# Kernel optimization log

Measured on AMD Instinct MI355X. Metric: run time of the kernel, lower is better.

## Reference

```python
import jax, jax.numpy as jnp
import numpy as np

H = 8          # n_heads
C_FACTOR = 3   # autocorrelation factor c
KS = 25        # series-decomp moving-average kernel


def series_decomp(x, ks=KS):
    # AvgPool1d(kernel=ks, stride=1, pad=ks//2), count_include_pad=True (torch default)
    p = ks // 2
    xp = jnp.pad(x, ((0, 0), (p, p), (0, 0)))            # [B, L+2p, D]
    cs = jnp.pad(jnp.cumsum(xp, axis=1), ((0, 0), (1, 0), (0, 0)))
    trend = (cs[:, ks:, :] - cs[:, :-ks, :]) / ks         # [B, L, D]
    return x - trend, trend


def auto_correlation(x, Wq, bq, Wk, bk, Wv, bv):
    B, L, D = x.shape
    d = D // H

    def proj(W, b):  # [B,L,D] -> [B,H,L,d]
        return (x @ W + b).reshape(B, L, H, d).transpose(0, 2, 1, 3)

    Q, K, V = proj(Wq, bq), proj(Wk, bk), proj(Wv, bv)
    Qf = jnp.fft.rfft(Q, axis=2)
    Kf = jnp.fft.rfft(K, axis=2)
    Corr = jnp.fft.irfft(Qf * jnp.conj(Kf), n=L, axis=2)  # [B,H,L,d]

    k = int(C_FACTOR * np.log(L))                         # topk = int(c*log(L))
    C2 = Corr.transpose(0, 1, 3, 2)                       # [B,H,d,L] - topk along lag axis per channel
    W_topk, I_topk = jax.lax.top_k(C2, k)                 # [B,H,d,k]
    W_topk = jax.nn.softmax(W_topk, axis=-1)

    # saturating shift: pos = min(delay + t, L-1)  (faithful to clamp(max=L-1))
    t = jnp.arange(L)
    pos = jnp.minimum(I_topk[..., None] + t[None, None, None, None, :], L - 1)  # [B,H,d,k,L]
    Vt = V.transpose(0, 1, 3, 2)                          # [B,H,d,L]
    gathered = jnp.take_along_axis(Vt[:, :, :, None, :], pos, axis=4)           # [B,H,d,k,L]
    R = jnp.einsum('bhdk,bhdkl->bhdl', W_topk, gathered)  # weighted aggregate over lags
    return R.transpose(0, 3, 1, 2).reshape(B, L, D)       # [B,L,D]


def setup_inputs() -> dict:
    key = jax.random.key(0)
    ks = jax.random.split(key, 11)
    B, L, D = 8, 1024, 512
    s = 0.02
    return {
        'x':  jax.random.normal(ks[0], (B, L, D), jnp.float32),
        'Wq': jax.random.normal(ks[1], (D, D), jnp.float32) * s,
        'bq': jnp.zeros((D,), jnp.float32),
        'Wk': jax.random.normal(ks[2], (D, D), jnp.float32) * s,
        'bk': jnp.zeros((D,), jnp.float32),
        'Wv': jax.random.normal(ks[3], (D, D), jnp.float32) * s,
        'bv': jnp.zeros((D,), jnp.float32),
        'W1': jax.random.normal(ks[4], (D, D), jnp.float32) * s,
        'b1': jnp.zeros((D,), jnp.float32),
        'W2': jax.random.normal(ks[5], (D, D), jnp.float32) * s,
        'b2': jnp.zeros((D,), jnp.float32),
    }


def reference(x, Wq, bq, Wk, bk, Wv, bv, W1, b1, W2, b2):
    attn = auto_correlation(x, Wq, bq, Wk, bk, Wv, bv)
    x_s, _ = series_decomp(attn + x)
    y = jax.nn.relu(x_s @ W1 + b1) @ W2 + b2              # FFN (dropout is identity in eval)
    x_s, _ = series_decomp(y + x_s)
    return x_s
```

## Files before the change

### kernel.cpp

```cpp
#include <hip/hip_runtime.h>
#include <math.h>

#define LL 1024
#define DD 512
#define NB 8
#define KTOP 20
#define SZ (8 * 512 * 1024)

typedef __attribute__((ext_vector_type(8))) short bf16x8;
typedef __attribute__((ext_vector_type(4))) float f32x4;
typedef __attribute__((ext_vector_type(4))) int i32x4;

__device__ __forceinline__ unsigned short f2bf(float f) {
  union { float f; unsigned u; } v; v.f = f;
  unsigned r = v.u + 0x7FFFu + ((v.u >> 16) & 1u);
  return (unsigned short)(r >> 16);
}
__device__ __forceinline__ float bf2f(unsigned short u) {
  union { unsigned u; float f; } v; v.u = ((unsigned)u) << 16;
  return v.f;
}

__device__ __forceinline__ void gload16(const void* g, void* l) {
  __builtin_amdgcn_global_load_lds(
      (const __attribute__((address_space(1))) unsigned int*)g,
      (__attribute__((address_space(3))) unsigned int*)l, 16, 0, 0);
}

__global__ __launch_bounds__(256) void k_prep(const float* __restrict__ x,
                                              unsigned short* __restrict__ xbT,
                                              unsigned short* __restrict__ xb,
                                              const float* __restrict__ Wq,
                                              const float* __restrict__ Wk,
                                              const float* __restrict__ Wv,
                                              const float* __restrict__ W1,
                                              const float* __restrict__ W2,
                                              const float* __restrict__ bq,
                                              const float* __restrict__ bk,
                                              const float* __restrict__ bv,
                                              unsigned short* __restrict__ WqkvT,
                                              unsigned short* __restrict__ W1T,
                                              unsigned short* __restrict__ W2T,
                                              float* __restrict__ bqkv) {
  __shared__ float T[64][65];
  int bid = blockIdx.x;
  int tid = threadIdx.x;
  int lane = tid & 63, r4 = tid >> 6;
  if (bid < 1024) {
    int b = bid >> 7, c0 = ((bid >> 4) & 7) * 64, t0 = (bid & 15) * 64;
#pragma unroll
    for (int it = 0; it < 16; ++it) {
      int tl = it * 4 + r4;
      T[lane][tl] = x[((size_t)b * LL + t0 + tl) * DD + c0 + lane];
    }
    __syncthreads();
#pragma unroll
    for (int it = 0; it < 16; ++it) {
      int cl = it * 4 + r4;
      xbT[((size_t)b * DD + c0 + cl) * LL + t0 + lane] = f2bf(T[cl][lane]);
    }
    int tl2 = tid >> 2, cq = (tid & 3) * 16;
    unsigned short* dxb = xb + ((size_t)b * LL + t0 + tl2) * DD + c0 + cq;
#pragma unroll
    for (int j = 0; j < 16; j += 4) {
      ushort4 u;
      u.x = f2bf(T[cq + j][tl2]);
      u.y = f2bf(T[cq + j + 1][tl2]);
      u.z = f2bf(T[cq + j + 2][tl2]);
      u.w = f2bf(T[cq + j + 3][tl2]);
      *(ushort4*)&dxb[j] = u;
    }
  } else {
    int pid = bid - 1024;
    int z = pid >> 6, n0 = ((pid >> 3) & 7) * 64, k0 = (pid & 7) * 64;
    const float* W = (z == 0) ? Wq : (z == 1) ? Wk : (z == 2) ? Wv : (z == 3) ? W1 : W2;
    unsigned short* dst = (z == 0) ? WqkvT
                        : (z == 1) ? (WqkvT + 512 * 512)
                        : (z == 2) ? (WqkvT + 1024 * 512)
                        : (z == 3) ? W1T : W2T;
#pragma unroll
    for (int it = 0; it < 16; ++it) {
      int kl = it * 4 + r4;
      T[lane][kl] = W[(size_t)(k0 + kl) * DD + n0 + lane];
    }
    __syncthreads();
    int n = tid >> 2, kq = (tid & 3) * 16;
    unsigned short* d = dst + (size_t)(n0 + n) * DD + k0 + kq;
#pragma unroll
    for (int j = 0; j < 16; j += 4) {
      ushort4 u;
      u.x = f2bf(T[n][kq + j]);
      u.y = f2bf(T[n][kq + j + 1]);
      u.z = f2bf(T[n][kq + j + 2]);
      u.w = f2bf(T[n][kq + j + 3]);
      *(ushort4*)&d[j] = u;
    }
    if (z == 4 && n0 == 0 && k0 == 0) {
      for (int i = tid; i < 1536; i += 256) {
        const float* s = (i < 512) ? bq : (i < 1024) ? bk : bv;
        bqkv[i] = s[i & 511];
      }
    }
  }
}

template <int MODE>
__global__ __launch_bounds__(256) void k_mfma(const unsigned short* __restrict__ Aptr,
                                              const unsigned short* __restrict__ Bt,
                                              const float* __restrict__ bias,
                                              const unsigned short* __restrict__ resbT,
                                              unsigned short* __restrict__ outU,
                                              float* __restrict__ outF, int gx) {
  __shared__ char smem[34816];
  unsigned short* As = (unsigned short*)smem;
  unsigned short* Bs = (unsigned short*)(smem + 16384);
  float* Cs = (float*)smem;

  int tid = threadIdx.x;
  int lane = tid & 63, wid = tid >> 6;
  int wr = wid & 1, wc = wid >> 1;

  int nwg = gridDim.x;
  int wg = blockIdx.x;
  int swz = (wg & 7) * (nwg >> 3) + (wg >> 3);
  int bix = swz % gx, biy = swz / gx;
  int n0 = bix * 128, m0 = biy * 128;
  int b = m0 >> 10, t0 = m0 & (LL - 1);

  f32x4 acc[4][4];
#pragma unroll
  for (int i = 0; i < 4; ++i)
#pragma unroll
    for (int j = 0; j < 4; ++j) acc[i][j] = (f32x4){0.f, 0.f, 0.f, 0.f};

  int srow = tid >> 3, sq = tid & 7;

  for (int k0 = 0; k0 < 512; k0 += 64) {
#pragma unroll
    for (int p = 0; p < 4; ++p) {
      int r = srow + p * 32;
      int dq = sq ^ (r & 7);
      gload16(Aptr + (size_t)(m0 + r) * 512 + k0 + dq * 8, &As[r * 64 + sq * 8]);
      gload16(Bt + (size_t)(n0 + r) * 512 + k0 + dq * 8, &Bs[r * 64 + sq * 8]);
    }
    __syncthreads();
#pragma unroll
    for (int ks = 0; ks < 2; ++ks) {
      bf16x8 af[4], bf[4];
      int fr = lane & 15, kq = lane >> 4;
#pragma unroll
      for (int mi = 0; mi < 4; ++mi) {
        int r = wr * 64 + mi * 16 + fr;
        af[mi] = *(bf16x8*)&As[r * 64 + ((ks * 4 + kq) ^ (r & 7)) * 8];
      }
#pragma unroll
      for (int ni = 0; ni < 4; ++ni) {
        int r = wc * 64 + ni * 16 + fr;
        bf[ni] = *(bf16x8*)&Bs[r * 64 + ((ks * 4 + kq) ^ (r & 7)) * 8];
      }
#pragma unroll
      for (int mi = 0; mi < 4; ++mi)
#pragma unroll
        for (int ni = 0; ni < 4; ++ni)
          acc[mi][ni] = __builtin_amdgcn_mfma_f32_16x16x32_bf16(af[mi], bf[ni], acc[mi][ni], 0, 0, 0);
    }
    __syncthreads();
  }

  if (MODE == 0 || MODE == 2) {
    const int LDc = 132;
    for (int p = 0; p < 2; ++p) {
      __syncthreads();
      if (MODE == 2) {
        int n = tid >> 2, mq = tid & 3;
        const unsigned short* rrow =
            resbT + ((size_t)(b * 512) + n0 + p * 64 + n) * LL + t0;
#pragma unroll
        for (int i = 0; i < 8; ++i) {
          int m = mq * 4 + i * 16;
          ushort4 u = *(const ushort4*)&rrow[m];
          float4 v;
          v.x = bf2f(u.x); v.y = bf2f(u.y); v.z = bf2f(u.z); v.w = bf2f(u.w);
          *(float4*)&Cs[n * LDc + m] = v;
        }
        __syncthreads();
      }
      if (wc == p) {
#pragma unroll
        for (int mi = 0; mi < 4; ++mi)
#pragma unroll
          for (int ni = 0; ni < 4; ++ni) {
            int nl = ni * 16 + (lane & 15);
            int ml = wr * 64 + mi * 16 + (lane >> 4) * 4;
            if (MODE == 2) {
              f32x4 cur = *(f32x4*)&Cs[nl * LDc + ml];
              cur += acc[mi][ni];
              *(f32x4*)&Cs[nl * LDc + ml] = cur;
            } else {
              *(f32x4*)&Cs[nl * LDc + ml] = acc[mi][ni];
            }
          }
      }
      __syncthreads();
      {
        int n = tid >> 2, mq = tid & 3;
        int ng = n0 + p * 64 + n;
        float bv = bias[ng];
        if (MODE == 0) {
          int sel = ng >> 9;
          unsigned short* drow =
              outU + ((size_t)sel * NB * 512 + b * 512 + (ng & 511)) * LL + t0;
#pragma unroll
          for (int i = 0; i < 8; ++i) {
            int m = mq * 4 + i * 16;
            float4 v = *(float4*)&Cs[n * LDc + m];
            ushort4 u;
            u.x = f2bf(v.x + bv); u.y = f2bf(v.y + bv);
            u.z = f2bf(v.z + bv); u.w = f2bf(v.w + bv);
            *(ushort4*)&drow[m] = u;
          }
        } else {
          float* drow = outF + ((size_t)b * 512 + ng) * LL + t0;
#pragma unroll
          for (int i = 0; i < 8; ++i) {
            int m = mq * 4 + i * 16;
            float4 v = *(float4*)&Cs[n * LDc + m];
            v.x += bv; v.y += bv; v.z += bv; v.w += bv;
            *(float4*)&drow[m] = v;
          }
        }
      }
    }
  } else {
    const int LDh = 68;
    for (int p = 0; p < 2; ++p) {
      __syncthreads();
      if (wc == p) {
#pragma unroll
        for (int mi = 0; mi < 4; ++mi)
#pragma unroll
          for (int ni = 0; ni < 4; ++ni) {
            int nl = ni * 16 + (lane & 15);
            int ml = wr * 64 + mi * 16 + (lane >> 4) * 4;
#pragma unroll
            for (int r = 0; r < 4; ++r) Cs[(ml + r) * LDh + nl] = acc[mi][ni][r];
          }
      }
      __syncthreads();
      {
        int m = tid >> 1, nh = tid & 1;
        unsigned short* drow =
            outU + (size_t)(m0 + m) * 512 + n0 + p * 64 + nh * 32;
#pragma unroll
        for (int c = 0; c < 8; ++c) {
          float4 v = *(float4*)&Cs[m * LDh + nh * 32 + c * 4];
          float4 bb = *(const float4*)&bias[n0 + p * 64 + nh * 32 + c * 4];
          v.x = fmaxf(v.x + bb.x, 0.f);
          v.y = fmaxf(v.y + bb.y, 0.f);
          v.z = fmaxf(v.z + bb.z, 0.f);
          v.w = fmaxf(v.w + bb.w, 0.f);
          ushort4 u;
          u.x = f2bf(v.x); u.y = f2bf(v.y); u.z = f2bf(v.z); u.w = f2bf(v.w);
          *(ushort4*)&drow[c * 4] = u;
        }
      }
    }
  }
}

__global__ __launch_bounds__(256, 8) void k_autocorr(const unsigned short* __restrict__ Qbf,
                                                     const unsigned short* __restrict__ Kbf,
                                                     const unsigned short* __restrict__ Vbf,
                                                     const unsigned short* __restrict__ xbT,
                                                     unsigned short* __restrict__ xsbT) {
  __shared__ char sm[16672];
  unsigned* KshW = (unsigned*)sm;
  float* Vs2 = (float*)(sm + 8320);
  float* wvs = (float*)(sm + 16512);
  int*   wis = (int*)(sm + 16592);
  float* Csp = (float*)sm;
  float* Cp  = (float*)(sm + 4224);

  int tid = threadIdx.x;
  int lane = tid & 63, wave = tid >> 6;
  size_t base = (size_t)blockIdx.x * LL;

  {
    ushort4 vv = *(const ushort4*)(Vbf + base + tid * 4);
    float4 vf;
    vf.x = bf2f(vv.x); vf.y = bf2f(vv.y); vf.z = bf2f(vv.z); vf.w = bf2f(vv.w);
    *(float4*)&Vs2[tid * 4] = vf;
    float vlast = bf2f(Vbf[base + 1023]);
    *(float4*)&Vs2[1024 + tid * 4] = make_float4(vlast, vlast, vlast, vlast);

    ushort4 kv = *(const ushort4*)(Kbf + base + tid * 4);
    unsigned w0 = (unsigned)kv.x | ((unsigned)kv.y << 16);
    unsigned w1 = (unsigned)kv.z | ((unsigned)kv.w << 16);
    unsigned wq = __shfl_up(w0, 1);
    unsigned wp = __shfl_up(w1, 1);
    if (lane == 0) {
      wq = *(const unsigned*)(Kbf + base + ((tid * 4 - 4) & (LL - 1)));
      wp = *(const unsigned*)(Kbf + base + ((tid * 4 - 2) & (LL - 1)));
    }
    int d = 8 + 2 * tid;
    uint2 u0; u0.x = w0;                      u0.y = w1;
    uint2 u1; u1.x = (wp >> 16) | (w0 << 16); u1.y = (w0 >> 16) | (w1 << 16);
    uint2 u2; u2.x = wp;                      u2.y = w0;
    uint2 u3; u3.x = (wq >> 16) | (wp << 16); u3.y = (wp >> 16) | (w0 << 16);
    *(uint2*)&KshW[d]        = u0;
    *(uint2*)&KshW[520 + d]  = u1;
    *(uint2*)&KshW[1040 + d] = u2;
    *(uint2*)&KshW[1560 + d] = u3;
    if (tid >= 224) {
      int q2 = tid - 224;
      int s = q2 >> 3, dd = q2 & 7;
      int p = 2 * dd - 16;
      unsigned short a = Kbf[base + ((p - s) & (LL - 1))];
      unsigned short b2 = Kbf[base + ((p + 1 - s) & (LL - 1))];
      KshW[s * 520 + dd] = (unsigned)a | ((unsigned)b2 << 16);
    }
  }
  __syncthreads();

  f32x4 acc = (f32x4){0.f, 0.f, 0.f, 0.f};
  int fr = lane & 15, kq = lane >> 4;
  int g = wave;
  int srow = fr & 3, fp = fr >> 2;
  int aE = (256 * g + 16 * fr + 8 * kq) & (LL - 1);
  int bD0 = srow * 520 + 8 + 4 * kq - 2 * fp;
  const unsigned short* qp = Qbf + base;
#pragma unroll
  for (int ks = 0; ks < 32; ++ks) {
    bf16x8 av = *(const bf16x8*)(qp + aE);
    int bD = bD0 + 16 * ks;
    uint2 b01 = *(const uint2*)&KshW[bD];
    uint2 b23 = *(const uint2*)&KshW[bD + 2];
    union { unsigned u[4]; bf16x8 h; } ub;
    ub.u[0] = b01.x; ub.u[1] = b01.y; ub.u[2] = b23.x; ub.u[3] = b23.y;
    acc = __builtin_amdgcn_mfma_f32_16x16x32_bf16(av, ub.h, acc, 0, 0, 0);
    aE = (aE + 32) & (LL - 1);
  }
  __syncthreads();
#pragma unroll
  for (int r = 0; r < 4; ++r) {
    int tau = 256 * g + 64 * kq + 16 * r + fr;
    Cp[tau ^ (((tau >> 6) & 3) << 4)] = acc[r];
  }
  __syncthreads();

  int sel = blockIdx.x & 3;
  if (wave == sel) {
    float c0[16];
#pragma unroll
    for (int j = 0; j < 16; ++j) {
      int tau = 64 * j + lane;
      c0[j] = Cp[tau ^ (((tau >> 6) & 3) << 4)];
    }
    float lbest = c0[0];
    int lidx = 0;
#pragma unroll
    for (int m = 1; m < 16; ++m)
      if (c0[m] > lbest) { lbest = c0[m]; lidx = m; }

#pragma unroll 1
    for (int s = 0; s < KTOP; ++s) {
      float best = lbest;
      int bidx = 64 * lidx + lane;
#pragma unroll
      for (int off = 32; off; off >>= 1) {
        float v2 = __shfl_xor(best, off);
        int i2 = __shfl_xor(bidx, off);
        if (v2 > best || (v2 == best && i2 < bidx)) { best = v2; bidx = i2; }
      }
      if (lane == 0) { wvs[s] = best; wis[s] = bidx; }
      int kill = ((bidx & 63) == lane) ? (bidx >> 6) : -1;
#pragma unroll
      for (int m = 0; m < 16; ++m)
        if (m == kill) c0[m] = -3.0e38f;
      lbest = c0[0];
      lidx = 0;
#pragma unroll
      for (int m = 1; m < 16; ++m)
        if (c0[m] > lbest) { lbest = c0[m]; lidx = m; }
    }
    float mx = wvs[0];
    float e = (lane < KTOP) ? __expf(wvs[lane] - mx) : 0.f;
    float ssum = e;
#pragma unroll
    for (int off = 32; off; off >>= 1) ssum += __shfl_xor(ssum, off);
    if (lane < KTOP) wvs[lane] = e / ssum;
  } else {
    int ft = (wave < sel ? wave : wave - 1) * 64 + lane;
    if (ft < 16) Csp[ft] = 0.f;
    else if (ft < 32) Csp[1040 + ft - 16] = 0.f;
  }
  __syncthreads();

  {
    float r[4];
#pragma unroll
    for (int i = 0; i < 4; ++i) r[i] = bf2f(xbT[base + tid + 256 * i]);
#pragma unroll
    for (int k = 0; k < KTOP; ++k) {
      float w = wvs[k];
      int wi = wis[k];
#pragma unroll
      for (int i = 0; i < 4; ++i) r[i] += w * Vs2[wi + tid + 256 * i];
    }
#pragma unroll
    for (int i = 0; i < 4; ++i) Csp[16 + tid + 256 * i] = r[i];
  }
  __syncthreads();

  {
    int t0 = tid * 4;
    float buf[28];
#pragma unroll
    for (int qd = 0; qd < 7; ++qd)
      *(float4*)&buf[qd * 4] = *(const float4*)&Csp[t0 + 4 + qd * 4];
    float s = 0.f;
#pragma unroll
    for (int m = 0; m < 25; ++m) s += buf[m];
    ushort4 o;
    o.x = f2bf(buf[12] - s * (1.0f / 25.0f));
    s += buf[25] - buf[0];
    o.y = f2bf(buf[13] - s * (1.0f / 25.0f));
    s += buf[26] - buf[1];
    o.z = f2bf(buf[14] - s * (1.0f / 25.0f));
    s += buf[27] - buf[2];
    o.w = f2bf(buf[15] - s * (1.0f / 25.0f));
    *(ushort4*)&xsbT[base + t0] = o;
  }
}

__global__ __launch_bounds__(256) void k_castT(const unsigned short* __restrict__ src,
                                               unsigned short* __restrict__ dst) {
  __shared__ unsigned short T[64][68];
  int b = blockIdx.z;
  int t0 = blockIdx.x * 64, c0 = blockIdx.y * 64;
  int tid = threadIdx.x;
  int lane = tid & 63, r4 = tid >> 6;
#pragma unroll
  for (int it = 0; it < 16; ++it) {
    int cl = it * 4 + r4;
    T[lane][cl] = src[((size_t)b * 512 + c0 + cl) * LL + t0 + lane];
  }
  __syncthreads();
  int tl = tid >> 2, cq = (tid & 3) * 16;
  unsigned short* d = dst + ((size_t)b * LL + t0 + tl) * 512 + c0 + cq;
#pragma unroll
  for (int j = 0; j < 16; j += 4) {
    ushort4 u;
    u.x = T[tl][cq + j]; u.y = T[tl][cq + j + 1];
    u.z = T[tl][cq + j + 2]; u.w = T[tl][cq + j + 3];
    *(ushort4*)&d[j] = u;
  }
}

#define DCH 32
__global__ __launch_bounds__(256) void k_decomp2T(const float* __restrict__ s2T,
                                                  float* __restrict__ out) {
  __shared__ float T[DCH][289];
  int b = blockIdx.z, c0 = blockIdx.y * DCH, t0 = blockIdx.x * 256;
  int tid = threadIdx.x;
  {
    int row = tid >> 3, j0 = tid & 7;
    const float* src = s2T + ((size_t)b * 512 + c0 + row) * LL;
#pragma unroll
    for (int i = 0; i < 9; ++i) {
      int col = (j0 + i * 8) * 4;
      int t = t0 - 16 + col;
      float4 v = make_float4(0.f, 0.f, 0.f, 0.f);
      if (t >= 0 && t < LL) v = *(const float4*)&src[t];
      *(float4*)&T[row][col] = v;
    }
  }
  __syncthreads();
  int c = tid & 31, tg = tid >> 5;
  float sum = 0.f;
  int basec = tg * 32 + 4;
#pragma unroll
  for (int j = 0; j < 25; ++j) sum += T[c][basec + j];
  float* orow = out + ((size_t)b * LL + t0 + tg * 32) * 512 + c0 + c;
#pragma unroll 1
  for (int s = 0; s < 32; ++s) {
    float center = T[c][tg * 32 + 16 + s];
    orow[(size_t)s * 512] = center - sum * (1.f / 25.f);
    sum += T[c][basec + 25 + s] - T[c][basec + s];
  }
}

extern "C" void kernel_launch(void* const* d_in, const int* in_sizes, int n_in,
                              void* d_out, int out_size, void* d_ws, size_t ws_size,
                              hipStream_t stream) {
  const float* x  = (const float*)d_in[0];
  const float* Wq = (const float*)d_in[1];
  const float* bq = (const float*)d_in[2];
  const float* Wk = (const float*)d_in[3];
  const float* bk = (const float*)d_in[4];
  const float* Wv = (const float*)d_in[5];
  const float* bv = (const float*)d_in[6];
  const float* W1 = (const float*)d_in[7];
  const float* b1 = (const float*)d_in[8];
  const float* W2 = (const float*)d_in[9];
  const float* b2 = (const float*)d_in[10];
  float* out = (float*)d_out;
  char* w = (char*)d_ws;

  unsigned short* xbT   = (unsigned short*)w;
  unsigned short* Qbf   = (unsigned short*)(w + (size_t)SZ * 4);
  unsigned short* Kbf   = Qbf + SZ;
  unsigned short* Vbf   = Kbf + SZ;
  unsigned short* WqkvT = (unsigned short*)(w + (size_t)SZ * 12);
  unsigned short* W1T   = WqkvT + 1536 * 512;
  unsigned short* W2T   = W1T + 512 * 512;
  float* bqkv           = (float*)(W2T + 512 * 512);
  unsigned short* xb    = (unsigned short*)(w + (size_t)SZ * 14);
  unsigned short* h1    = (unsigned short*)w;
  unsigned short* xsb   = (unsigned short*)(w + (size_t)SZ * 2);
  unsigned short* xsbT  = Qbf;
  float* s2T            = (float*)(w + (size_t)SZ * 6);

  k_prep<<<dim3(1344), 256, 0, stream>>>(x, xbT, xb, Wq, Wk, Wv, W1, W2,
                                         bq, bk, bv, WqkvT, W1T, W2T, bqkv);

  k_mfma<0><<<dim3(768), 256, 0, stream>>>(xb, WqkvT, bqkv, nullptr, Qbf, nullptr, 12);

  k_autocorr<<<dim3(NB * DD), 256, 0, stream>>>(Qbf, Kbf, Vbf, xbT, xsbT);

  k_castT<<<dim3(16, 8, NB), 256, 0, stream>>>(xsbT, xsb);

  k_mfma<1><<<dim3(256), 256, 0, stream>>>(xsb, W1T, b1, nullptr, h1, nullptr, 4);
  k_mfma<2><<<dim3(256), 256, 0, stream>>>(h1, W2T, b2, xsbT, nullptr, s2T, 4);

  k_decomp2T<<<dim3(4, 16, NB), 256, 0, stream>>>(s2T, out);
}
```

Measured before the change: 139.7 us.

## Halve FFN GEMM M-tile and shrink autocorr shifted-K staging

The GEMM kernel is templated on the M-tile size, and the two FFN GEMMs now use 64-row tiles with 512 workgroups instead of 256, to fill more compute units. The epilogue index mappings are adjusted to match. Separately, the autocorrelation kernel now stages only two shifted copies of K in shared memory instead of four, with a new B-fragment addressing scheme and a different LDS layout. This lets it drop one barrier and several shuffles and stores. Smaller tiles lower reuse per workgroup, and the new K indexing carries a correctness risk.

```diff
diff --git a/kernel.cpp b/kernel.cpp
--- a/kernel.cpp
+++ b/kernel.cpp
@@ -104,16 +104,17 @@
   }
 }
 
-template <int MODE>
+template <int MODE, int BM>
 __global__ __launch_bounds__(256) void k_mfma(const unsigned short* __restrict__ Aptr,
                                               const unsigned short* __restrict__ Bt,
                                               const float* __restrict__ bias,
                                               const unsigned short* __restrict__ resbT,
                                               unsigned short* __restrict__ outU,
                                               float* __restrict__ outF, int gx) {
-  __shared__ char smem[34816];
+  constexpr int MI = BM / 32;
+  __shared__ char smem[(BM + 128) * 64 * 2 + (BM == 128 ? 2048 : 0)];
   unsigned short* As = (unsigned short*)smem;
-  unsigned short* Bs = (unsigned short*)(smem + 16384);
+  unsigned short* Bs = (unsigned short*)(smem + BM * 128);
   float* Cs = (float*)smem;
 
   int tid = threadIdx.x;
@@ -124,33 +125,38 @@
   int wg = blockIdx.x;
   int swz = (wg & 7) * (nwg >> 3) + (wg >> 3);
   int bix = swz % gx, biy = swz / gx;
-  int n0 = bix * 128, m0 = biy * 128;
+  int n0 = bix * 128, m0 = biy * BM;
   int b = m0 >> 10, t0 = m0 & (LL - 1);
 
-  f32x4 acc[4][4];
-#pragma unroll
-  for (int i = 0; i < 4; ++i)
+  f32x4 acc[MI][4];
+#pragma unroll
+  for (int i = 0; i < MI; ++i)
 #pragma unroll
     for (int j = 0; j < 4; ++j) acc[i][j] = (f32x4){0.f, 0.f, 0.f, 0.f};
 
   int srow = tid >> 3, sq = tid & 7;
 
   for (int k0 = 0; k0 < 512; k0 += 64) {
+#pragma unroll
+    for (int p = 0; p < MI; ++p) {
+      int r = srow + p * 32;
+      int dq = sq ^ (r & 7);
+      gload16(Aptr + (size_t)(m0 + r) * 512 + k0 + dq * 8, &As[r * 64 + sq * 8]);
+    }
 #pragma unroll
     for (int p = 0; p < 4; ++p) {
       int r = srow + p * 32;
       int dq = sq ^ (r & 7);
-      gload16(Aptr + (size_t)(m0 + r) * 512 + k0 + dq * 8, &As[r * 64 + sq * 8]);
       gload16(Bt + (size_t)(n0 + r) * 512 + k0 + dq * 8, &Bs[r * 64 + sq * 8]);
     }
     __syncthreads();
 #pragma unroll
     for (int ks = 0; ks < 2; ++ks) {
-      bf16x8 af[4], bf[4];
+      bf16x8 af[MI], bf[4];
       int fr = lane & 15, kq = lane >> 4;
 #pragma unroll
-      for (int mi = 0; mi < 4; ++mi) {
-        int r = wr * 64 + mi * 16 + fr;
+      for (int mi = 0; mi < MI; ++mi) {
+        int r = wr * (BM / 2) + mi * 16 + fr;
         af[mi] = *(bf16x8*)&As[r * 64 + ((ks * 4 + kq) ^ (r & 7)) * 8];
       }
 #pragma unroll
@@ -159,7 +165,7 @@
         bf[ni] = *(bf16x8*)&Bs[r * 64 + ((ks * 4 + kq) ^ (r & 7)) * 8];
       }
 #pragma unroll
-      for (int mi = 0; mi < 4; ++mi)
+      for (int mi = 0; mi < MI; ++mi)
 #pragma unroll
         for (int ni = 0; ni < 4; ++ni)
           acc[mi][ni] = __builtin_amdgcn_mfma_f32_16x16x32_bf16(af[mi], bf[ni], acc[mi][ni], 0, 0, 0);
@@ -167,38 +173,67 @@
     __syncthreads();
   }
 
-  if (MODE == 0 || MODE == 2) {
+  if (MODE == 0) {
     const int LDc = 132;
     for (int p = 0; p < 2; ++p) {
       __syncthreads();
-      if (MODE == 2) {
+      if (wc == p) {
+#pragma unroll
+        for (int mi = 0; mi < MI; ++mi)
+#pragma unroll
+          for (int ni = 0; ni < 4; ++ni) {
+            int nl = ni * 16 + (lane & 15);
+            int ml = wr * (BM / 2) + mi * 16 + (lane >> 4) * 4;
+            *(f32x4*)&Cs[nl * LDc + ml] = acc[mi][ni];
+          }
+      }
+      __syncthreads();
+      {
+        int n = tid >> 2, mq = tid & 3;
+        int ng = n0 + p * 64 + n;
+        float bv = bias[ng];
+        int sel = ng >> 9;
+        unsigned short* drow =
+            outU + ((size_t)sel * NB * 512 + b * 512 + (ng & 511)) * LL + t0;
+#pragma unroll
+        for (int i = 0; i < 8; ++i) {
+          int m = mq * 4 + i * 16;
+          float4 v = *(float4*)&Cs[n * LDc + m];
+          ushort4 u;
+          u.x = f2bf(v.x + bv); u.y = f2bf(v.y + bv);
+          u.z = f2bf(v.z + bv); u.w = f2bf(v.w + bv);
+          *(ushort4*)&drow[m] = u;
+        }
+      }
+    }
+  } else if (MODE == 2) {
+    const int LDc = 68;
+    for (int p = 0; p < 2; ++p) {
+      __syncthreads();
+      {
         int n = tid >> 2, mq = tid & 3;
         const unsigned short* rrow =
             resbT + ((size_t)(b * 512) + n0 + p * 64 + n) * LL + t0;
 #pragma unroll
-        for (int i = 0; i < 8; ++i) {
-          int m = mq * 4 + i * 16;
+        for (int i = 0; i < 4; ++i) {
+          int m = mq * 16 + i * 4;
           ushort4 u = *(const ushort4*)&rrow[m];
           float4 v;
           v.x = bf2f(u.x); v.y = bf2f(u.y); v.z = bf2f(u.z); v.w = bf2f(u.w);
           *(float4*)&Cs[n * LDc + m] = v;
         }
-        __syncthreads();
-      }
+      }
+      __syncthreads();
       if (wc == p) {
 #pragma unroll
-        for (int mi = 0; mi < 4; ++mi)
+        for (int mi = 0; mi < MI; ++mi)
 #pragma unroll
           for (int ni = 0; ni < 4; ++ni) {
             int nl = ni * 16 + (lane & 15);
-            int ml = wr * 64 + mi * 16 + (lane >> 4) * 4;
-            if (MODE == 2) {
-              f32x4 cur = *(f32x4*)&Cs[nl * LDc + ml];
-              cur += acc[mi][ni];
-              *(f32x4*)&Cs[nl * LDc + ml] = cur;
-            } else {
-              *(f32x4*)&Cs[nl * LDc + ml] = acc[mi][ni];
-            }
+            int ml = wr * (BM / 2) + mi * 16 + (lane >> 4) * 4;
+            f32x4 cur = *(f32x4*)&Cs[nl * LDc + ml];
+            cur += acc[mi][ni];
+            *(f32x4*)&Cs[nl * LDc + ml] = cur;
           }
       }
       __syncthreads();
@@ -206,28 +241,13 @@
         int n = tid >> 2, mq = tid & 3;
         int ng = n0 + p * 64 + n;
         float bv = bias[ng];
-        if (MODE == 0) {
-          int sel = ng >> 9;
-          unsigned short* drow =
-              outU + ((size_t)sel * NB * 512 + b * 512 + (ng & 511)) * LL + t0;
-#pragma unroll
-          for (int i = 0; i < 8; ++i) {
-            int m = mq * 4 + i * 16;
-            float4 v = *(float4*)&Cs[n * LDc + m];
-            ushort4 u;
-            u.x = f2bf(v.x + bv); u.y = f2bf(v.y + bv);
-            u.z = f2bf(v.z + bv); u.w = f2bf(v.w + bv);
-            *(ushort4*)&drow[m] = u;
-          }
-        } else {
-          float* drow = outF + ((size_t)b * 512 + ng) * LL + t0;
-#pragma unroll
-          for (int i = 0; i < 8; ++i) {
-            int m = mq * 4 + i * 16;
-            float4 v = *(float4*)&Cs[n * LDc + m];
-            v.x += bv; v.y += bv; v.z += bv; v.w += bv;
-            *(float4*)&drow[m] = v;
-          }
+        float* drow = outF + ((size_t)b * 512 + ng) * LL + t0;
+#pragma unroll
+        for (int i = 0; i < 4; ++i) {
+          int m = mq * 16 + i * 4;
+          float4 v = *(float4*)&Cs[n * LDc + m];
+          v.x += bv; v.y += bv; v.z += bv; v.w += bv;
+          *(float4*)&drow[m] = v;
         }
       }
     }
@@ -237,24 +257,24 @@
       __syncthreads();
       if (wc == p) {
 #pragma unroll
-        for (int mi = 0; mi < 4; ++mi)
+        for (int mi = 0; mi < MI; ++mi)
 #pragma unroll
           for (int ni = 0; ni < 4; ++ni) {
             int nl = ni * 16 + (lane & 15);
-            int ml = wr * 64 + mi * 16 + (lane >> 4) * 4;
+            int ml = wr * (BM / 2) + mi * 16 + (lane >> 4) * 4;
 #pragma unroll
             for (int r = 0; r < 4; ++r) Cs[(ml + r) * LDh + nl] = acc[mi][ni][r];
           }
       }
       __syncthreads();
       {
-        int m = tid >> 1, nh = tid & 1;
+        int m = tid >> 2, nh = tid & 3;
         unsigned short* drow =
-            outU + (size_t)(m0 + m) * 512 + n0 + p * 64 + nh * 32;
-#pragma unroll
-        for (int c = 0; c < 8; ++c) {
-          float4 v = *(float4*)&Cs[m * LDh + nh * 32 + c * 4];
-          float4 bb = *(const float4*)&bias[n0 + p * 64 + nh * 32 + c * 4];
+            outU + (size_t)(m0 + m) * 512 + n0 + p * 64 + nh * 16;
+#pragma unroll
+        for (int c = 0; c < 4; ++c) {
+          float4 v = *(float4*)&Cs[m * LDh + nh * 16 + c * 4];
+          float4 bb = *(const float4*)&bias[n0 + p * 64 + nh * 16 + c * 4];
           v.x = fmaxf(v.x + bb.x, 0.f);
           v.y = fmaxf(v.y + bb.y, 0.f);
           v.z = fmaxf(v.z + bb.z, 0.f);
@@ -274,12 +294,12 @@
                                                      const unsigned short* __restrict__ xbT,
                                                      unsigned short* __restrict__ xsbT) {
   __shared__ char sm[16672];
-  unsigned* KshW = (unsigned*)sm;
+  float* Cp  = (float*)sm;
+  unsigned* KshW = (unsigned*)(sm + 4096);
+  float* Csp = (float*)(sm + 4096);
   float* Vs2 = (float*)(sm + 8320);
   float* wvs = (float*)(sm + 16512);
   int*   wis = (int*)(sm + 16592);
-  float* Csp = (float*)sm;
-  float* Cp  = (float*)(sm + 4224);
 
   int tid = threadIdx.x;
   int lane = tid & 63, wave = tid >> 6;
@@ -296,28 +316,24 @@
     ushort4 kv = *(const ushort4*)(Kbf + base + tid * 4);
     unsigned w0 = (unsigned)kv.x | ((unsigned)kv.y << 16);
     unsigned w1 = (unsigned)kv.z | ((unsigned)kv.w << 16);
-    unsigned wq = __shfl_up(w0, 1);
     unsigned wp = __shfl_up(w1, 1);
-    if (lane == 0) {
-      wq = *(const unsigned*)(Kbf + base + ((tid * 4 - 4) & (LL - 1)));
+    if (lane == 0)
       wp = *(const unsigned*)(Kbf + base + ((tid * 4 - 2) & (LL - 1)));
-    }
     int d = 8 + 2 * tid;
     uint2 u0; u0.x = w0;                      u0.y = w1;
     uint2 u1; u1.x = (wp >> 16) | (w0 << 16); u1.y = (w0 >> 16) | (w1 << 16);
-    uint2 u2; u2.x = wp;                      u2.y = w0;
-    uint2 u3; u3.x = (wq >> 16) | (wp << 16); u3.y = (wp >> 16) | (w0 << 16);
-    *(uint2*)&KshW[d]        = u0;
-    *(uint2*)&KshW[520 + d]  = u1;
-    *(uint2*)&KshW[1040 + d] = u2;
-    *(uint2*)&KshW[1560 + d] = u3;
-    if (tid >= 224) {
+    *(uint2*)&KshW[d]       = u0;
+    *(uint2*)&KshW[528 + d] = u1;
+    if (tid >= 224 && tid < 240) {
       int q2 = tid - 224;
-      int s = q2 >> 3, dd = q2 & 7;
-      int p = 2 * dd - 16;
-      unsigned short a = Kbf[base + ((p - s) & (LL - 1))];
-      unsigned short b2 = Kbf[base + ((p + 1 - s) & (LL - 1))];
-      KshW[s * 520 + dd] = (unsigned)a | ((unsigned)b2 << 16);
+      if (q2 < 8) {
+        KshW[q2] = *(const unsigned*)(Kbf + base + 1008 + 2 * q2);
+      } else {
+        int dd = q2 - 8;
+        unsigned short a = Kbf[base + 1007 + 2 * dd];
+        unsigned short b2 = Kbf[base + 1008 + 2 * dd];
+        KshW[528 + dd] = (unsigned)a | ((unsigned)b2 << 16);
+      }
     }
   }
   __syncthreads();
@@ -325,9 +341,8 @@
   f32x4 acc = (f32x4){0.f, 0.f, 0.f, 0.f};
   int fr = lane & 15, kq = lane >> 4;
   int g = wave;
-  int srow = fr & 3, fp = fr >> 2;
   int aE = (256 * g + 16 * fr + 8 * kq) & (LL - 1);
-  int bD0 = srow * 520 + 8 + 4 * kq - 2 * fp;
+  int bD0 = (fr & 1) * 528 + 8 + 4 * kq - (fr >> 1);
   const unsigned short* qp = Qbf + base;
 #pragma unroll
   for (int ks = 0; ks < 32; ++ks) {
@@ -340,7 +355,6 @@
     acc = __builtin_amdgcn_mfma_f32_16x16x32_bf16(av, ub.h, acc, 0, 0, 0);
     aE = (aE + 32) & (LL - 1);
   }
-  __syncthreads();
 #pragma unroll
   for (int r = 0; r < 4; ++r) {
     int tau = 256 * g + 64 * kq + 16 * r + fr;
@@ -524,14 +538,14 @@
   k_prep<<<dim3(1344), 256, 0, stream>>>(x, xbT, xb, Wq, Wk, Wv, W1, W2,
                                          bq, bk, bv, WqkvT, W1T, W2T, bqkv);
 
-  k_mfma<0><<<dim3(768), 256, 0, stream>>>(xb, WqkvT, bqkv, nullptr, Qbf, nullptr, 12);
+  k_mfma<0, 128><<<dim3(768), 256, 0, stream>>>(xb, WqkvT, bqkv, nullptr, Qbf, nullptr, 12);
 
   k_autocorr<<<dim3(NB * DD), 256, 0, stream>>>(Qbf, Kbf, Vbf, xbT, xsbT);
 
   k_castT<<<dim3(16, 8, NB), 256, 0, stream>>>(xsbT, xsb);
 
-  k_mfma<1><<<dim3(256), 256, 0, stream>>>(xsb, W1T, b1, nullptr, h1, nullptr, 4);
-  k_mfma<2><<<dim3(256), 256, 0, stream>>>(h1, W2T, b2, xsbT, nullptr, s2T, 4);
+  k_mfma<1, 64><<<dim3(512), 256, 0, stream>>>(xsb, W1T, b1, nullptr, h1, nullptr, 4);
+  k_mfma<2, 64><<<dim3(512), 256, 0, stream>>>(h1, W2T, b2, xsbT, nullptr, s2T, 4);
 
   k_decomp2T<<<dim3(4, 16, NB), 256, 0, stream>>>(s2T, out);
 }
```

After: 229.4 us. 1.64x slower.
